# Kernel optimization log

Measured on AMD Instinct MI355X. Metric: run time of the kernel, lower is better.

Reference implementation:

```python
import jax, jax.numpy as jnp
import numpy as np

BLOCK_SIZE = 3
SOBEL_PAD = 1  # sobel_size // 2
BLOCK_PAD = BLOCK_SIZE // 2

_SOBEL_X = jnp.array([[-1.0, 0.0, 1.0], [-2.0, 0.0, 2.0], [-1.0, 0.0, 1.0]], dtype=jnp.float32)[None, None]
_SOBEL_Y = jnp.array([[-1.0, -2.0, -1.0], [0.0, 0.0, 0.0], [1.0, 2.0, 1.0]], dtype=jnp.float32)[None, None]
_SUM_K = jnp.ones((1, 1, BLOCK_SIZE, BLOCK_SIZE), dtype=jnp.float32)


def _pad_replicate(x, p):
    return jnp.pad(x, ((0, 0), (0, 0), (p, p), (p, p)), mode='edge')


def _conv(x, k):
    return jax.lax.conv_general_dilated(
        x, k, window_strides=(1, 1), padding='VALID',
        dimension_numbers=('NCHW', 'OIHW', 'NCHW'))


def setup_inputs() -> dict:
    key = jax.random.key(0)
    image = jax.random.uniform(key, (8, 1, 1080, 1920), dtype=jnp.float32) * 255.0
    return {"image": image}


def reference(image) -> jnp.ndarray:
    img = image.astype(jnp.float32)
    img_p = _pad_replicate(img, SOBEL_PAD)
    Ix = _conv(img_p, _SOBEL_X)
    Iy = _conv(img_p, _SOBEL_Y)
    Ixx = Ix * Ix
    Iyy = Iy * Iy
    Ixy = Ix * Iy
    sum_Ixx = _conv(_pad_replicate(Ixx, BLOCK_PAD), _SUM_K)
    sum_Iyy = _conv(_pad_replicate(Iyy, BLOCK_PAD), _SUM_K)
    sum_Ixy = _conv(_pad_replicate(Ixy, BLOCK_PAD), _SUM_K)
    half_trace = (sum_Ixx + sum_Iyy) * 0.5
    diff_half = (sum_Ixx - sum_Iyy) * 0.5
    sqrt_disc = jnp.sqrt(diff_half * diff_half + sum_Ixy * sum_Ixy + 1e-10)
    lambda_min = half_trace - sqrt_disc
    return jnp.clip(lambda_min, 0.0)
```

## Files before the change

### kernel.cpp

```cpp
#include <hip/hip_runtime.h>

#define IMG_H 1080
#define IMG_W 1920
#define NBATCH 8

__global__ __launch_bounds__(256, 4)
void shi_tomasi_kernel(const float* __restrict__ img, float* __restrict__ out) {
    const int cg    = threadIdx.x & 31;
    const int strip = threadIdx.x >> 5;
    const int vb = blockIdx.x * 128 + cg * 4;
    const int s0 = blockIdx.y * 72 + strip * 9;
    const int b  = blockIdx.z;
    const float* g = img + (size_t)b * (IMG_H * IMG_W);

    const bool eL = (vb == 0);
    const bool eR = (vb == IMG_W - 4);
    const int  o0 = eL ? 0 : (eR ? vb - 4 : vb - 2);
    const bool topFix = (s0 == 0);
    const bool botFix = (s0 + 9 == IMG_H);

    float hdR[3][6], hsR[3][6], hfd[3], hfs[3], h[3][12];

    auto load_row = [&](int lr, float* hd, float* hs, float& fd, float& fs) {
        const float* rp = g + (size_t)lr * IMG_W + o0;
        const float2 p0 = *(const float2*)(rp);
        const float2 p1 = *(const float2*)(rp + 2);
        const float2 p2 = *(const float2*)(rp + 4);
        const float2 p3 = *(const float2*)(rp + 6);
        float z0=p0.x, z1=p0.y, z2=p1.x, z3=p1.y, z4=p2.x, z5=p2.y, z6=p3.x, z7=p3.y;
        if (eL) { z7=z5; z6=z4; z5=z3; z4=z2; z3=z1; z2=z0; z1=z0; }
        if (eR) { z0=z2; z1=z3; z2=z4; z3=z5; z4=z6; z5=z7; z6=z7; }
        hd[0]=z2-z0; hd[1]=z3-z1; hd[2]=z4-z2; hd[3]=z5-z3; hd[4]=z6-z4; hd[5]=z7-z5;
        hs[0]=z0+2.0f*z1+z2; hs[1]=z1+2.0f*z2+z3; hs[2]=z2+2.0f*z3+z4;
        hs[3]=z3+2.0f*z4+z5; hs[4]=z4+2.0f*z5+z6; hs[5]=z5+2.0f*z6+z7;
        fd = eR ? (z5-z4) : (z3-z2);
        fs = eR ? (z4+3.0f*z5) : (3.0f*z2+z3);
    };

    load_row(max(s0-2,0), hdR[0], hsR[0], hfd[0], hfs[0]);
    load_row(max(s0-1,0), hdR[1], hsR[1], hfd[1], hfs[1]);

    float* orow = out + ((size_t)b * IMG_H + s0) * IMG_W + vb;

    #pragma unroll
    for (int rr = 0; rr < 11; ++rr) {
        const int sm = rr % 3;
        const int sz = (rr + 1) % 3;
        const int sp = (rr + 2) % 3;
        load_row(min(s0 + rr, IMG_H - 1), hdR[sp], hsR[sp], hfd[sp], hfs[sp]);

        float Ix[6], Iy[6];
        #pragma unroll
        for (int t = 0; t < 6; ++t) {
            Ix[t] = hdR[sm][t] + 2.0f * hdR[sz][t] + hdR[sp][t];
            Iy[t] = hsR[sp][t] - hsR[sm][t];
        }
        const float ixf = hfd[sm] + 2.0f * hfd[sz] + hfd[sp];
        const float iyf = hfs[sp] - hfs[sm];
        if (eL) { Ix[0] = ixf; Iy[0] = iyf; }
        if (eR) { Ix[5] = ixf; Iy[5] = iyf; }

        float pxx[6], pyy[6], pxy[6];
        #pragma unroll
        for (int t = 0; t < 6; ++t) {
            pxx[t] = Ix[t] * Ix[t];
            pyy[t] = Iy[t] * Iy[t];
            pxy[t] = Ix[t] * Iy[t];
        }
        float* hr = h[rr % 3];
        #pragma unroll
        for (int o = 0; o < 4; ++o) {
            hr[o]     = pxx[o] + pxx[o+1] + pxx[o+2];
            hr[4 + o] = pyy[o] + pyy[o+1] + pyy[o+2];
            hr[8 + o] = pxy[o] + pxy[o+1] + pxy[o+2];
        }
        if (rr == 1) {
            #pragma unroll
            for (int q = 0; q < 12; ++q) if (topFix) h[0][q] = hr[q];
        }
        if (rr == 10) {
            const float* hprev = h[(rr - 1) % 3];
            #pragma unroll
            for (int q = 0; q < 12; ++q) if (botFix) hr[q] = hprev[q];
        }

        if (rr >= 2) {
            const float* h0 = h[(rr - 2) % 3];
            const float* h1 = h[(rr - 1) % 3];
            const float* h2 = h[rr % 3];
            float rv[4];
            #pragma unroll
            for (int o = 0; o < 4; ++o) {
                const float sxx = h0[o]     + h1[o]     + h2[o];
                const float syy = h0[4 + o] + h1[4 + o] + h2[4 + o];
                const float sxy = h0[8 + o] + h1[8 + o] + h2[8 + o];
                const float ht   = 0.5f * (sxx + syy);
                const float dh   = 0.5f * (sxx - syy);
                const float disc = fmaf(dh, dh, fmaf(sxy, sxy, 1e-10f));
                rv[o] = fmaxf(ht - sqrtf(disc), 0.0f);
            }
            *(float4*)orow = make_float4(rv[0], rv[1], rv[2], rv[3]);
            orow += IMG_W;
        }
    }
}

extern "C" void kernel_launch(void* const* d_in, const int* in_sizes, int n_in,
                              void* d_out, int out_size, void* d_ws, size_t ws_size,
                              hipStream_t stream) {
    const float* img = (const float*)d_in[0];
    float* out = (float*)d_out;
    dim3 grid(IMG_W / 128, IMG_H / 72, NBATCH);
    shi_tomasi_kernel<<<grid, 256, 0, stream>>>(img, out);
}
```

Baseline: 125.4 us.

## Software-pipeline row loads four rows ahead with raw register ring buffer

Row loads are split from their use: raw pixel rows are issued four iterations ahead into a five-entry register ring, and the horizontal Sobel and structure-tensor work runs on rows already loaded. Loads also change from four float2 accesses to two 8-byte-aligned 16-byte accesses, and launch bounds drop from 4 to 3 blocks per SIMD to make room for the extra live registers. The aim is to hide global memory latency inside each thread. The cost is higher register pressure and possibly lower occupancy.

```diff
diff --git a/kernel.cpp b/kernel.cpp
--- a/kernel.cpp
+++ b/kernel.cpp
@@ -4,7 +4,9 @@
 #define IMG_W 1920
 #define NBATCH 8
 
-__global__ __launch_bounds__(256, 4)
+struct __attribute__((aligned(8))) f4u { float a, b, c, d; };
+
+__global__ __launch_bounds__(256, 3)
 void shi_tomasi_kernel(const float* __restrict__ img, float* __restrict__ out) {
     const int cg    = threadIdx.x & 31;
     const int strip = threadIdx.x >> 5;
@@ -19,88 +21,101 @@
     const bool topFix = (s0 == 0);
     const bool botFix = (s0 + 9 == IMG_H);
 
+    float raw[5][8];
     float hdR[3][6], hsR[3][6], hfd[3], hfs[3], h[3][12];
 
-    auto load_row = [&](int lr, float* hd, float* hs, float& fd, float& fs) {
+    auto issue = [&](int k) {
+        int lr = s0 - 2 + k; lr = max(0, min(IMG_H - 1, lr));
         const float* rp = g + (size_t)lr * IMG_W + o0;
-        const float2 p0 = *(const float2*)(rp);
-        const float2 p1 = *(const float2*)(rp + 2);
-        const float2 p2 = *(const float2*)(rp + 4);
-        const float2 p3 = *(const float2*)(rp + 6);
-        float z0=p0.x, z1=p0.y, z2=p1.x, z3=p1.y, z4=p2.x, z5=p2.y, z6=p3.x, z7=p3.y;
-        if (eL) { z7=z5; z6=z4; z5=z3; z4=z2; z3=z1; z2=z0; z1=z0; }
-        if (eR) { z0=z2; z1=z3; z2=z4; z3=z5; z4=z6; z5=z7; z6=z7; }
-        hd[0]=z2-z0; hd[1]=z3-z1; hd[2]=z4-z2; hd[3]=z5-z3; hd[4]=z6-z4; hd[5]=z7-z5;
-        hs[0]=z0+2.0f*z1+z2; hs[1]=z1+2.0f*z2+z3; hs[2]=z2+2.0f*z3+z4;
-        hs[3]=z3+2.0f*z4+z5; hs[4]=z4+2.0f*z5+z6; hs[5]=z5+2.0f*z6+z7;
-        fd = eR ? (z5-z4) : (z3-z2);
-        fs = eR ? (z4+3.0f*z5) : (3.0f*z2+z3);
+        const f4u va = *(const f4u*)rp;
+        const f4u vc = *(const f4u*)(rp + 4);
+        float* r = raw[k % 5];
+        r[0] = va.a; r[1] = va.b; r[2] = va.c; r[3] = va.d;
+        r[4] = vc.a; r[5] = vc.b; r[6] = vc.c; r[7] = vc.d;
     };
 
-    load_row(max(s0-2,0), hdR[0], hsR[0], hfd[0], hfs[0]);
-    load_row(max(s0-1,0), hdR[1], hsR[1], hfd[1], hfs[1]);
+    #pragma unroll
+    for (int k = 0; k < 4; ++k) issue(k);
 
     float* orow = out + ((size_t)b * IMG_H + s0) * IMG_W + vb;
 
     #pragma unroll
-    for (int rr = 0; rr < 11; ++rr) {
-        const int sm = rr % 3;
-        const int sz = (rr + 1) % 3;
-        const int sp = (rr + 2) % 3;
-        load_row(min(s0 + rr, IMG_H - 1), hdR[sp], hsR[sp], hfd[sp], hfs[sp]);
+    for (int k = 0; k < 13; ++k) {
+        if (k + 4 < 13) issue(k + 4);
 
-        float Ix[6], Iy[6];
-        #pragma unroll
-        for (int t = 0; t < 6; ++t) {
-            Ix[t] = hdR[sm][t] + 2.0f * hdR[sz][t] + hdR[sp][t];
-            Iy[t] = hsR[sp][t] - hsR[sm][t];
-        }
-        const float ixf = hfd[sm] + 2.0f * hfd[sz] + hfd[sp];
-        const float iyf = hfs[sp] - hfs[sm];
-        if (eL) { Ix[0] = ixf; Iy[0] = iyf; }
-        if (eR) { Ix[5] = ixf; Iy[5] = iyf; }
-
-        float pxx[6], pyy[6], pxy[6];
-        #pragma unroll
-        for (int t = 0; t < 6; ++t) {
-            pxx[t] = Ix[t] * Ix[t];
-            pyy[t] = Iy[t] * Iy[t];
-            pxy[t] = Ix[t] * Iy[t];
-        }
-        float* hr = h[rr % 3];
-        #pragma unroll
-        for (int o = 0; o < 4; ++o) {
-            hr[o]     = pxx[o] + pxx[o+1] + pxx[o+2];
-            hr[4 + o] = pyy[o] + pyy[o+1] + pyy[o+2];
-            hr[8 + o] = pxy[o] + pxy[o+1] + pxy[o+2];
-        }
-        if (rr == 1) {
-            #pragma unroll
-            for (int q = 0; q < 12; ++q) if (topFix) h[0][q] = hr[q];
-        }
-        if (rr == 10) {
-            const float* hprev = h[(rr - 1) % 3];
-            #pragma unroll
-            for (int q = 0; q < 12; ++q) if (botFix) hr[q] = hprev[q];
+        {
+            const float* r = raw[k % 5];
+            float z0=r[0], z1=r[1], z2=r[2], z3=r[3], z4=r[4], z5=r[5], z6=r[6], z7=r[7];
+            if (eL) { z7=z5; z6=z4; z5=z3; z4=z2; z3=z1; z2=z0; z1=z0; }
+            if (eR) { z0=z2; z1=z3; z2=z4; z3=z5; z4=z6; z5=z7; z6=z7; }
+            float* hd = hdR[k % 3];
+            float* hs = hsR[k % 3];
+            hd[0]=z2-z0; hd[1]=z3-z1; hd[2]=z4-z2; hd[3]=z5-z3; hd[4]=z6-z4; hd[5]=z7-z5;
+            hs[0]=z0+2.0f*z1+z2; hs[1]=z1+2.0f*z2+z3; hs[2]=z2+2.0f*z3+z4;
+            hs[3]=z3+2.0f*z4+z5; hs[4]=z4+2.0f*z5+z6; hs[5]=z5+2.0f*z6+z7;
+            hfd[k % 3] = eR ? (z5-z4) : (z3-z2);
+            hfs[k % 3] = eR ? (z4+3.0f*z5) : (3.0f*z2+z3);
         }
 
-        if (rr >= 2) {
-            const float* h0 = h[(rr - 2) % 3];
-            const float* h1 = h[(rr - 1) % 3];
-            const float* h2 = h[rr % 3];
-            float rv[4];
+        if (k >= 2) {
+            const int rr = k - 2;
+            const int sm = rr % 3;
+            const int sz = (rr + 1) % 3;
+            const int sp = (rr + 2) % 3;
+
+            float Ix[6], Iy[6];
+            #pragma unroll
+            for (int t = 0; t < 6; ++t) {
+                Ix[t] = hdR[sm][t] + 2.0f * hdR[sz][t] + hdR[sp][t];
+                Iy[t] = hsR[sp][t] - hsR[sm][t];
+            }
+            const float ixf = hfd[sm] + 2.0f * hfd[sz] + hfd[sp];
+            const float iyf = hfs[sp] - hfs[sm];
+            if (eL) { Ix[0] = ixf; Iy[0] = iyf; }
+            if (eR) { Ix[5] = ixf; Iy[5] = iyf; }
+
+            float pxx[6], pyy[6], pxy[6];
+            #pragma unroll
+            for (int t = 0; t < 6; ++t) {
+                pxx[t] = Ix[t] * Ix[t];
+                pyy[t] = Iy[t] * Iy[t];
+                pxy[t] = Ix[t] * Iy[t];
+            }
+            float* hr = h[rr % 3];
             #pragma unroll
             for (int o = 0; o < 4; ++o) {
-                const float sxx = h0[o]     + h1[o]     + h2[o];
-                const float syy = h0[4 + o] + h1[4 + o] + h2[4 + o];
-                const float sxy = h0[8 + o] + h1[8 + o] + h2[8 + o];
-                const float ht   = 0.5f * (sxx + syy);
-                const float dh   = 0.5f * (sxx - syy);
-                const float disc = fmaf(dh, dh, fmaf(sxy, sxy, 1e-10f));
-                rv[o] = fmaxf(ht - sqrtf(disc), 0.0f);
+                hr[o]     = pxx[o] + pxx[o+1] + pxx[o+2];
+                hr[4 + o] = pyy[o] + pyy[o+1] + pyy[o+2];
+                hr[8 + o] = pxy[o] + pxy[o+1] + pxy[o+2];
             }
-            *(float4*)orow = make_float4(rv[0], rv[1], rv[2], rv[3]);
-            orow += IMG_W;
+            if (rr == 1) {
+                #pragma unroll
+                for (int q = 0; q < 12; ++q) if (topFix) h[0][q] = hr[q];
+            }
+            if (rr == 10) {
+                const float* hprev = h[(rr - 1) % 3];
+                #pragma unroll
+                for (int q = 0; q < 12; ++q) if (botFix) hr[q] = hprev[q];
+            }
+
+            if (rr >= 2) {
+                const float* h0 = h[(rr - 2) % 3];
+                const float* h1 = h[(rr - 1) % 3];
+                const float* h2 = hr;
+                float rv[4];
+                #pragma unroll
+                for (int o = 0; o < 4; ++o) {
+                    const float sxx = h0[o]     + h1[o]     + h2[o];
+                    const float syy = h0[4 + o] + h1[4 + o] + h2[4 + o];
+                    const float sxy = h0[8 + o] + h1[8 + o] + h2[8 + o];
+                    const float ht   = 0.5f * (sxx + syy);
+                    const float dh   = 0.5f * (sxx - syy);
+                    const float disc = fmaf(dh, dh, fmaf(sxy, sxy, 1e-10f));
+                    rv[o] = fmaxf(ht - sqrtf(disc), 0.0f);
+                }
+                *(float4*)orow = make_float4(rv[0], rv[1], rv[2], rv[3]);
+                orow += IMG_W;
+            }
         }
     }
 }
```

After: 121.9 us. -2.8%, faster.
